# Optimization experiments

Hardware: AMD Instinct MI355X
Metric: run time of the kernel (lower is better)

The kernel has to match this reference:

```python
import jax, jax.numpy as jnp
import numpy as np

H, N, M = 1024, 128, 512
EPS_COS = 1e-8


def setup_inputs() -> dict:
    key = jax.random.key(0)
    ks = iter(jax.random.split(key, 64))
    def rn(shape, s=0.02):
        return jax.random.normal(next(ks), shape, jnp.float32) * s
    x = jax.random.normal(next(ks), (1, H), jnp.float32)
    prw = jax.random.uniform(next(ks), (1, N), jnp.float32)
    prev_read_w = prw / jnp.sum(prw, axis=1, keepdims=True)
    pww = jax.random.uniform(next(ks), (1, N), jnp.float32)
    prev_write_w = pww / jnp.sum(pww, axis=1, keepdims=True)
    inp = {
        "x": x,
        "prev_read_w": prev_read_w,
        "prev_write_w": prev_write_w,
        "h0": rn((1, H), 0.1),
        "c0": rn((1, H), 0.1),
        "memory": jnp.ones((N, M), jnp.float32),
        "W_ih": rn((4 * H, H)), "W_hh": rn((4 * H, H)),
        "b_ih": rn((4 * H,)), "b_hh": rn((4 * H,)),
        "rk_w": rn((M, H)), "rk_b": rn((M,)),
        "rbeta_w": rn((1, H)), "rbeta_b": rn((1,)),
        "rg_w": rn((1, H)), "rg_b": rn((1,)),
        "rs_w": rn((N, H)), "rs_b": rn((N,)),
        "rgamma_w": rn((1, H)), "rgamma_b": rn((1,)),
        "wk_w": rn((M, H)), "wk_b": rn((M,)),
        "wbeta_w": rn((1, H)), "wbeta_b": rn((1,)),
        "wg_w": rn((1, H)), "wg_b": rn((1,)),
        "ws_w": rn((N, H)), "ws_b": rn((N,)),
        "wgamma_w": rn((1, H)), "wgamma_b": rn((1,)),
        "we_w": rn((N * M, H)), "we_b": rn((N * M,)),
        "wa_w": rn((M, H)), "wa_b": rn((M,)),
        "fc_w": rn((H, H + M)), "fc_b": rn((H,)),
    }
    return inp


def _lstm_cell(x, h, c, W_ih, W_hh, b_ih, b_hh):
    # torch gate order: i, f, g, o
    gates = x @ W_ih.T + b_ih + h @ W_hh.T + b_hh  # (1, 4H)
    i, f, g, o = jnp.split(gates, 4, axis=1)
    c_new = jax.nn.sigmoid(f) * c + jax.nn.sigmoid(i) * jnp.tanh(g)
    h_new = jax.nn.sigmoid(o) * jnp.tanh(c_new)
    return h_new, c_new


def _address(x, prev_w, mem, k_w, k_b, beta_w, beta_b, g_w, g_b, s_w, s_b, gamma_w, gamma_b):
    k = x @ k_w.T + k_b                                  # (1, M)
    beta = jax.nn.softplus(x @ beta_w.T + beta_b)        # (1, 1)
    g = jax.nn.sigmoid(x @ g_w.T + g_b)                  # (1, 1)
    s = jax.nn.softmax(x @ s_w.T + s_b, axis=-1)         # (1, N)
    gamma = 1.0 + jax.nn.softplus(x @ gamma_w.T + gamma_b)  # (1, 1)
    # cosine similarity of each memory row with k
    mem_n = jnp.maximum(jnp.linalg.norm(mem, axis=1), EPS_COS)     # (N,)
    k_n = jnp.maximum(jnp.linalg.norm(k[0]), EPS_COS)
    cos = (mem @ k[0]) / (mem_n * k_n)                   # (N,)
    w_c = jax.nn.softmax(beta * cos[None, :], axis=1)    # (1, N)
    w_g = g * w_c + (1.0 - g) * prev_w                   # (1, N)
    # circular convolution: w_t[i] = sum_j w_g[j] * s[(i - j) mod N]
    idx = (jnp.arange(N)[:, None] - jnp.arange(N)[None, :]) % N    # (N, N)
    w_t = (s[0][idx] @ w_g[0])[None, :]                  # (1, N)
    w = w_t ** gamma
    w = w / (jnp.sum(w, axis=1, keepdims=True) + 1e-16)
    return w


def reference(x, prev_read_w, prev_write_w, h0, c0, memory,
              W_ih, W_hh, b_ih, b_hh,
              rk_w, rk_b, rbeta_w, rbeta_b, rg_w, rg_b, rs_w, rs_b, rgamma_w, rgamma_b,
              wk_w, wk_b, wbeta_w, wbeta_b, wg_w, wg_b, ws_w, ws_b, wgamma_w, wgamma_b,
              we_w, we_b, wa_w, wa_b, fc_w, fc_b):
    sg = jax.lax.stop_gradient
    # controller (single LSTM step, batch 1)
    h, c = _lstm_cell(x, h0, c0, W_ih, W_hh, b_ih, b_hh)
    co = h  # controller output (1, H)
    mem = sg(memory)  # memory is detached in the original
    # read head
    rw = _address(co, prev_read_w, mem, rk_w, rk_b, rbeta_w, rbeta_b,
                  rg_w, rg_b, rs_w, rs_b, rgamma_w, rgamma_b)
    read = rw @ mem                                      # (1, M)
    # write head (note: receives prev_read_w, faithful to source)
    ww = _address(co, prev_read_w, mem, wk_w, wk_b, wbeta_w, wbeta_b,
                  wg_w, wg_b, ws_w, ws_b, wgamma_w, wgamma_b)
    e = jax.nn.sigmoid(co @ we_w.T + we_b)               # (1, N*M)
    a = co @ wa_w.T + wa_b                               # (1, M)
    # memory write with detached w, e, a (as in original)
    ww_d, e_d, a_d = sg(ww), sg(e), sg(a)
    new_mem = memory * (1.0 - ww_d @ e_d.reshape(N, M))  # (1,M) broadcast over (N,M)
    new_mem = new_mem + ww_d.T * a_d                     # (N,1)*(1,M)
    # output projection
    fc_in = jnp.concatenate([co, read], axis=1)          # (1, H+M)
    out = fc_in @ fc_w.T + fc_b                          # (1, H)
    return (out, sg(rw), sg(ww), h, c, new_mem)
```

## Files before the change

kernel.cpp:

```cpp
#include <hip/hip_runtime.h>
#include <math.h>

#define HH 1024
#define NN 128
#define MM 512

typedef float vf4 __attribute__((ext_vector_type(4)));

#define OFF_RW 1024
#define OFF_WW 1152
#define OFF_H  1280
#define OFF_C  2304
#define OFF_NM 3328

#define WS_GATES   0
#define WS_MNORM   5120
#define WS_A       5248
#define WS_KR      5760
#define WS_KW      6272
#define WS_RSLOG   6784
#define WS_WSLOG   6912
#define WS_FCPART  7040
#define WS_SCAL    8064
#define WS_WWV     8072
#define WS_RWV     8200
#define WS_ERASE   8328
#define WS_READ    8840

__device__ __forceinline__ float sigmoidf_(float z) { return 1.f / (1.f + expf(-z)); }
__device__ __forceinline__ float softplusf_(float z) {
    return fmaxf(z, 0.f) + log1pf(expf(-fabsf(z)));
}
__device__ __forceinline__ float wave_reduce(float v) {
    #pragma unroll
    for (int off = 32; off > 0; off >>= 1) v += __shfl_down(v, off, 64);
    return v;
}
__device__ __forceinline__ float wave_reduce_max(float v) {
    #pragma unroll
    for (int off = 32; off > 0; off >>= 1) v = fmaxf(v, __shfl_down(v, off, 64));
    return v;
}
__device__ __forceinline__ float block_sum(float v, float* wred, int t) {
    __syncthreads();
    float r = wave_reduce(v);
    if ((t & 63) == 0) wred[t >> 6] = r;
    __syncthreads();
    float s = 0.f;
    #pragma unroll
    for (int i = 0; i < 16; ++i) s += wred[i];
    return s;
}
__device__ __forceinline__ float block_max(float v, float* wred, int t) {
    __syncthreads();
    float r = wave_reduce_max(v);
    if ((t & 63) == 0) wred[t >> 6] = r;
    __syncthreads();
    float s = -1e30f;
    #pragma unroll
    for (int i = 0; i < 16; ++i) s = fmaxf(s, wred[i]);
    return s;
}

__device__ __forceinline__ void recompute_co(
    const float* __restrict__ gates, const float* __restrict__ c0,
    float* s_co, float* __restrict__ out, bool wr, int t)
{
    #pragma unroll
    for (int jj = 0; jj < 4; ++jj) {
        int j = t + jj * 256;
        float gi = gates[j], gf = gates[j + 1024];
        float gg = gates[j + 2048], go = gates[j + 3072];
        float cn = sigmoidf_(gf) * c0[j] + sigmoidf_(gi) * tanhf(gg);
        float hn = sigmoidf_(go) * tanhf(cn);
        s_co[j] = hn;
        if (wr) { out[OFF_H + j] = hn; out[OFF_C + j] = cn; }
    }
    __syncthreads();
}

__global__ __launch_bounds__(256) void k1_gates_norms(
    const float* __restrict__ x, const float* __restrict__ h0,
    const float* __restrict__ W_ih, const float* __restrict__ W_hh,
    const float* __restrict__ b_ih, const float* __restrict__ b_hh,
    const float* __restrict__ memory, float* __restrict__ gates,
    float* __restrict__ mem_norm)
{
    int t = threadIdx.x, lane = t & 63, wv = t >> 6;
    if (blockIdx.x < 1024) {
        int r = blockIdx.x * 4 + wv;
        const vf4* wi = (const vf4*)(W_ih + (long long)r * HH);
        const vf4* wh = (const vf4*)(W_hh + (long long)r * HH);
        const vf4* x4 = (const vf4*)x;
        const vf4* h4 = (const vf4*)h0;
        float acc = 0.f;
        #pragma unroll
        for (int q = 0; q < 4; ++q) {
            vf4 aa = __builtin_nontemporal_load(&wi[q * 64 + lane]);
            vf4 bb = x4[q * 64 + lane];
            acc += aa[0] * bb[0] + aa[1] * bb[1] + aa[2] * bb[2] + aa[3] * bb[3];
        }
        #pragma unroll
        for (int q = 0; q < 4; ++q) {
            vf4 aa = __builtin_nontemporal_load(&wh[q * 64 + lane]);
            vf4 bb = h4[q * 64 + lane];
            acc += aa[0] * bb[0] + aa[1] * bb[1] + aa[2] * bb[2] + aa[3] * bb[3];
        }
        acc = wave_reduce(acc);
        if (lane == 0) gates[r] = acc + b_ih[r] + b_hh[r];
    } else {
        int n = (blockIdx.x - 1024) * 4 + wv;
        const vf4* r4 = (const vf4*)(memory + n * MM);
        float acc = 0.f;
        #pragma unroll
        for (int q = 0; q < 2; ++q) {
            vf4 aa = r4[q * 64 + lane];
            acc += aa[0] * aa[0] + aa[1] * aa[1] + aa[2] * aa[2] + aa[3] * aa[3];
        }
        acc = wave_reduce(acc);
        if (lane == 0) mem_norm[n] = sqrtf(acc);
    }
}

#define K3S_ROWS 2822
__global__ __launch_bounds__(256) void k3_small(
    const float* __restrict__ gates, const float* __restrict__ c0,
    const float* __restrict__ wa_w, const float* __restrict__ wa_b,
    const float* __restrict__ rk_w, const float* __restrict__ rk_b,
    const float* __restrict__ wk_w, const float* __restrict__ wk_b,
    const float* __restrict__ rs_w, const float* __restrict__ rs_b,
    const float* __restrict__ sw_w, const float* __restrict__ sw_b,
    const float* __restrict__ fc_w, const float* __restrict__ fc_b,
    const float* __restrict__ rbeta_w, const float* __restrict__ rbeta_b,
    const float* __restrict__ rg_w, const float* __restrict__ rg_b,
    const float* __restrict__ rgamma_w, const float* __restrict__ rgamma_b,
    const float* __restrict__ wbeta_w, const float* __restrict__ wbeta_b,
    const float* __restrict__ wg_w, const float* __restrict__ wg_b,
    const float* __restrict__ wgamma_w, const float* __restrict__ wgamma_b,
    float* __restrict__ a, float* __restrict__ kr, float* __restrict__ kw,
    float* __restrict__ rs_logit, float* __restrict__ ws_logit,
    float* __restrict__ fc_part, float* __restrict__ scal,
    float* __restrict__ out, float* __restrict__ erase)
{
    __shared__ float s_co[1024];
    int t = threadIdx.x, lane = t & 63, wv = t >> 6;
    bool b0 = (blockIdx.x == 0);
    recompute_co(gates, c0, s_co, out, b0, t);
    if (b0) { erase[t] = 0.f; erase[t + 256] = 0.f; }

    int r = blockIdx.x * 4 + wv;
    if (r >= K3S_ROWS) return;
    const float* row;
    float bias = 0.f;
    float* dst;
    if (r < 512) {
        row = wa_w + (long long)r * HH; if (lane == 0) bias = wa_b[r]; dst = a + r;
    } else if (r < 1024) {
        int i = r - 512; row = rk_w + (long long)i * HH; if (lane == 0) bias = rk_b[i]; dst = kr + i;
    } else if (r < 1536) {
        int i = r - 1024; row = wk_w + (long long)i * HH; if (lane == 0) bias = wk_b[i]; dst = kw + i;
    } else if (r < 1664) {
        int i = r - 1536; row = rs_w + (long long)i * HH; if (lane == 0) bias = rs_b[i]; dst = rs_logit + i;
    } else if (r < 1792) {
        int i = r - 1664; row = sw_w + (long long)i * HH; if (lane == 0) bias = sw_b[i]; dst = ws_logit + i;
    } else if (r < 2816) {
        int i = r - 1792; row = fc_w + (long long)i * 1536; if (lane == 0) bias = fc_b[i]; dst = fc_part + i;
    } else {
        int i = r - 2816;
        const float* wsrc; const float* bsrc;
        switch (i) {
            case 0: wsrc = rbeta_w;  bsrc = rbeta_b;  break;
            case 1: wsrc = rg_w;     bsrc = rg_b;     break;
            case 2: wsrc = rgamma_w; bsrc = rgamma_b; break;
            case 3: wsrc = wbeta_w;  bsrc = wbeta_b;  break;
            case 4: wsrc = wg_w;     bsrc = wg_b;     break;
            default: wsrc = wgamma_w; bsrc = wgamma_b; break;
        }
        row = wsrc; if (lane == 0) bias = bsrc[0]; dst = scal + i;
    }
    const vf4* r4 = (const vf4*)row;
    const vf4* c4 = (const vf4*)s_co;
    float acc = 0.f;
    #pragma unroll
    for (int q = 0; q < 4; ++q) {
        vf4 aa = r4[q * 64 + lane], bb = c4[q * 64 + lane];
        acc += aa[0] * bb[0] + aa[1] * bb[1] + aa[2] * bb[2] + aa[3] * bb[3];
    }
    acc = wave_reduce(acc);
    if (lane == 0) *dst = acc + bias;
}

__global__ __launch_bounds__(1024) void k4_address(
    const float* __restrict__ kr, const float* __restrict__ kw,
    const float* __restrict__ scal,
    const float* __restrict__ rs_logit, const float* __restrict__ ws_logit,
    const float* __restrict__ prev_w, const float* __restrict__ mem_norm,
    const float* __restrict__ memory,
    float* __restrict__ out, float* __restrict__ rwv, float* __restrict__ wwv)
{
    int head = blockIdx.x;
    int t = threadIdx.x, lane = t & 63, wv = t >> 6;
    const float* k = head ? kw : kr;
    const float* slog = head ? ws_logit : rs_logit;
    float beta  = softplusf_(scal[head ? 3 : 0]);
    float gg    = sigmoidf_(scal[head ? 4 : 1]);
    float gamma = 1.f + softplusf_(scal[head ? 5 : 2]);

    __shared__ float wred[16];
    __shared__ float s_cos[128];
    __shared__ float s_s[128];
    __shared__ float s_wg[128];

    float kv = (t < 512) ? k[t] : 0.f;
    float k_norm = sqrtf(block_sum(kv * kv, wred, t));

    const vf4* k4p = (const vf4*)k;
    vf4 bb0 = k4p[lane], bb1 = k4p[64 + lane];
    #pragma unroll
    for (int i = 0; i < 8; ++i) {
        int n = wv * 8 + i;
        const vf4* r4 = (const vf4*)(memory + n * MM);
        vf4 a0 = r4[lane], a1 = r4[64 + lane];
        float acc = a0[0] * bb0[0] + a0[1] * bb0[1] + a0[2] * bb0[2] + a0[3] * bb0[3]
                  + a1[0] * bb1[0] + a1[1] * bb1[1] + a1[2] * bb1[2] + a1[3] * bb1[3];
        acc = wave_reduce(acc);
        if (lane == 0)
            s_cos[n] = acc / (fmaxf(mem_norm[n], 1e-8f) * fmaxf(k_norm, 1e-8f));
    }
    __syncthreads();

    float z = (t < 128) ? beta * s_cos[t] : -1e30f;
    float zmax = block_max(z, wred, t);
    float ez = (t < 128) ? expf(z - zmax) : 0.f;
    float zsum = block_sum(ez, wred, t);
    if (t < 128) s_wg[t] = gg * (ez / zsum) + (1.f - gg) * prev_w[t];

    float sl = (t < 128) ? slog[t] : -1e30f;
    float smax = block_max(sl, wred, t);
    float es = (t < 128) ? expf(sl - smax) : 0.f;
    float ssum = block_sum(es, wred, t);
    if (t < 128) s_s[t] = es / ssum;
    __syncthreads();

    float wt = 0.f;
    if (t < 128) {
        #pragma unroll 8
        for (int j = 0; j < 128; ++j) wt += s_wg[j] * s_s[(t - j) & 127];
        wt = powf(wt, gamma);
    }
    float wsum = block_sum((t < 128) ? wt : 0.f, wred, t);
    if (t < 128) {
        float wf = wt / (wsum + 1e-16f);
        out[(head ? OFF_WW : OFF_RW) + t] = wf;
        (head ? wwv : rwv)[t] = wf;
    }
}

__global__ __launch_bounds__(256) void k5_bige(
    const float* __restrict__ gates, const float* __restrict__ c0,
    const float* __restrict__ we_w, const float* __restrict__ we_b,
    const float* __restrict__ wwv, float* __restrict__ erase,
    const float* __restrict__ rwv, const float* __restrict__ memory,
    float* __restrict__ readv)
{
    __shared__ float s_co[1024];
    int t = threadIdx.x, lane = t & 63, wv = t >> 6;
    int b = blockIdx.x;
    if (b < 4096) {
        recompute_co(gates, c0, s_co, (float*)0, false, t);
        int wid = b * 4 + wv;
        long long r0 = (long long)wid * 4;
        const vf4* c4 = (const vf4*)s_co;
        const float* base = we_w + r0 * HH;
        float acc0 = 0.f, acc1 = 0.f, acc2 = 0.f, acc3 = 0.f;
        #pragma unroll
        for (int q = 0; q < 4; ++q) {
            vf4 bb = c4[q * 64 + lane];
            vf4 a0 = __builtin_nontemporal_load((const vf4*)(base) + q * 64 + lane);
            vf4 a1 = __builtin_nontemporal_load((const vf4*)(base + HH) + q * 64 + lane);
            vf4 a2 = __builtin_nontemporal_load((const vf4*)(base + 2 * HH) + q * 64 + lane);
            vf4 a3 = __builtin_nontemporal_load((const vf4*)(base + 3 * HH) + q * 64 + lane);
            acc0 += a0[0] * bb[0] + a0[1] * bb[1] + a0[2] * bb[2] + a0[3] * bb[3];
            acc1 += a1[0] * bb[0] + a1[1] * bb[1] + a1[2] * bb[2] + a1[3] * bb[3];
            acc2 += a2[0] * bb[0] + a2[1] * bb[1] + a2[2] * bb[2] + a2[3] * bb[3];
            acc3 += a3[0] * bb[0] + a3[1] * bb[1] + a3[2] * bb[2] + a3[3] * bb[3];
        }
        acc0 = wave_reduce(acc0);
        acc1 = wave_reduce(acc1);
        acc2 = wave_reduce(acc2);
        acc3 = wave_reduce(acc3);
        if (lane == 0) {
            int n = (int)(r0 >> 9), m0 = (int)(r0 & 511);
            float wn = wwv[n];
            float e0 = sigmoidf_(acc0 + we_b[r0]);
            float e1 = sigmoidf_(acc1 + we_b[r0 + 1]);
            float e2 = sigmoidf_(acc2 + we_b[r0 + 2]);
            float e3 = sigmoidf_(acc3 + we_b[r0 + 3]);
            atomicAdd(&erase[m0],     wn * e0);
            atomicAdd(&erase[m0 + 1], wn * e1);
            atomicAdd(&erase[m0 + 2], wn * e2);
            atomicAdd(&erase[m0 + 3], wn * e3);
        }
    } else {
        if (t < 128) s_co[t] = rwv[t];
        __syncthreads();
        int m = (b - 4096) * 256 + t;
        float acc = 0.f;
        #pragma unroll 4
        for (int n = 0; n < NN; ++n) acc += s_co[n] * memory[n * MM + m];
        readv[m] = acc;
    }
}

__global__ __launch_bounds__(256) void k6_final(
    const float* __restrict__ memory, const float* __restrict__ erase,
    const float* __restrict__ wwv, const float* __restrict__ a,
    const float* __restrict__ fc_w, const float* __restrict__ fc_part,
    const float* __restrict__ readv, float* __restrict__ out)
{
    int b = blockIdx.x, t = threadIdx.x;
    if (b < 256) {
        int idx = b * 256 + t;
        int n = idx >> 9, m = idx & 511;
        out[OFF_NM + idx] = memory[idx] * (1.f - erase[m]) + wwv[n] * a[m];
    } else {
        int w = (b - 256) * 4 + (t >> 6);
        int lane = t & 63;
        const vf4* r4 = (const vf4*)(fc_w + (long long)w * 1536 + 1024);
        const vf4* v4 = (const vf4*)readv;
        float acc = 0.f;
        #pragma unroll
        for (int q = 0; q < 2; ++q) {
            vf4 aa = r4[q * 64 + lane], bb = v4[q * 64 + lane];
            acc += aa[0] * bb[0] + aa[1] * bb[1] + aa[2] * bb[2] + aa[3] * bb[3];
        }
        acc = wave_reduce(acc);
        if (lane == 0) out[w] = fc_part[w] + acc;
    }
}

extern "C" void kernel_launch(void* const* d_in, const int* in_sizes, int n_in,
                              void* d_out, int out_size, void* d_ws, size_t ws_size,
                              hipStream_t stream)
{
    const float* x           = (const float*)d_in[0];
    const float* prev_read_w = (const float*)d_in[1];
    const float* h0      = (const float*)d_in[3];
    const float* c0      = (const float*)d_in[4];
    const float* memory  = (const float*)d_in[5];
    const float* W_ih    = (const float*)d_in[6];
    const float* W_hh    = (const float*)d_in[7];
    const float* b_ih    = (const float*)d_in[8];
    const float* b_hh    = (const float*)d_in[9];
    const float* rk_w    = (const float*)d_in[10];
    const float* rk_b    = (const float*)d_in[11];
    const float* rbeta_w = (const float*)d_in[12];
    const float* rbeta_b = (const float*)d_in[13];
    const float* rg_w    = (const float*)d_in[14];
    const float* rg_b    = (const float*)d_in[15];
    const float* rs_w    = (const float*)d_in[16];
    const float* rs_b    = (const float*)d_in[17];
    const float* rgamma_w = (const float*)d_in[18];
    const float* rgamma_b = (const float*)d_in[19];
    const float* wk_w    = (const float*)d_in[20];
    const float* wk_b    = (const float*)d_in[21];
    const float* wbeta_w = (const float*)d_in[22];
    const float* wbeta_b = (const float*)d_in[23];
    const float* wg_w    = (const float*)d_in[24];
    const float* wg_b    = (const float*)d_in[25];
    const float* sw_w    = (const float*)d_in[26];
    const float* sw_b    = (const float*)d_in[27];
    const float* wgamma_w = (const float*)d_in[28];
    const float* wgamma_b = (const float*)d_in[29];
    const float* we_w    = (const float*)d_in[30];
    const float* we_b    = (const float*)d_in[31];
    const float* wa_w    = (const float*)d_in[32];
    const float* wa_b    = (const float*)d_in[33];
    const float* fc_w    = (const float*)d_in[34];
    const float* fc_b    = (const float*)d_in[35];

    float* ws  = (float*)d_ws;
    float* out = (float*)d_out;

    float* gates    = ws + WS_GATES;
    float* mem_norm = ws + WS_MNORM;
    float* a        = ws + WS_A;
    float* kr       = ws + WS_KR;
    float* kw       = ws + WS_KW;
    float* rs_logit = ws + WS_RSLOG;
    float* ws_logit = ws + WS_WSLOG;
    float* fc_part  = ws + WS_FCPART;
    float* scal     = ws + WS_SCAL;
    float* wwv      = ws + WS_WWV;
    float* rwv      = ws + WS_RWV;
    float* erase    = ws + WS_ERASE;
    float* readv    = ws + WS_READ;

    k1_gates_norms<<<1056, 256, 0, stream>>>(x, h0, W_ih, W_hh, b_ih, b_hh,
                                             memory, gates, mem_norm);
    k3_small<<<(K3S_ROWS + 3) / 4, 256, 0, stream>>>(
        gates, c0, wa_w, wa_b, rk_w, rk_b, wk_w, wk_b, rs_w, rs_b, sw_w, sw_b,
        fc_w, fc_b,
        rbeta_w, rbeta_b, rg_w, rg_b, rgamma_w, rgamma_b,
        wbeta_w, wbeta_b, wg_w, wg_b, wgamma_w, wgamma_b,
        a, kr, kw, rs_logit, ws_logit, fc_part, scal, out, erase);
    k4_address<<<2, 1024, 0, stream>>>(kr, kw, scal, rs_logit, ws_logit,
                                       prev_read_w, mem_norm, memory,
                                       out, rwv, wwv);
    k5_bige<<<4098, 256, 0, stream>>>(gates, c0, we_w, we_b, wwv, erase,
                                      rwv, memory, readv);
    k6_final<<<512, 256, 0, stream>>>(memory, erase, wwv, a, fc_w, fc_part,
                                      readv, out);
}
```

Measured before the change: 473.1 us.

## Fuse addressing into erase GEMV kernel and store erase vector instead of atomics

The addressing computation now runs as two extra blocks inside the big erase GEMV kernel, which removes the separate k4 launch. The controller output is written once to workspace, so the 4096 erase blocks no longer recompute the LSTM cell. The erase values e are stored in full (N*M) and reduced against ww in the final kernel, which also computes the read vector and the fc read projection, removing the atomics and one launch. In exchange the final kernel reads 256KB of e per block across 128 blocks, and the read/fc blocks each redundantly recompute the read vector.

```diff
diff --git a/kernel.cpp b/kernel.cpp
--- a/kernel.cpp
+++ b/kernel.cpp
@@ -14,6 +14,7 @@
 #define OFF_NM 3328
 
 #define WS_GATES   0
+#define WS_CO      4096
 #define WS_MNORM   5120
 #define WS_A       5248
 #define WS_KR      5760
@@ -24,8 +25,7 @@
 #define WS_SCAL    8064
 #define WS_WWV     8072
 #define WS_RWV     8200
-#define WS_ERASE   8328
-#define WS_READ    8840
+#define WS_E       8320
 
 __device__ __forceinline__ float sigmoidf_(float z) { return 1.f / (1.f + expf(-z)); }
 __device__ __forceinline__ float softplusf_(float z) {
@@ -41,42 +41,19 @@
     for (int off = 32; off > 0; off >>= 1) v = fmaxf(v, __shfl_down(v, off, 64));
     return v;
 }
-__device__ __forceinline__ float block_sum(float v, float* wred, int t) {
+__device__ __forceinline__ float block_sum4(float v, float* wred, int t) {
     __syncthreads();
     float r = wave_reduce(v);
     if ((t & 63) == 0) wred[t >> 6] = r;
     __syncthreads();
-    float s = 0.f;
-    #pragma unroll
-    for (int i = 0; i < 16; ++i) s += wred[i];
-    return s;
-}
-__device__ __forceinline__ float block_max(float v, float* wred, int t) {
+    return wred[0] + wred[1] + wred[2] + wred[3];
+}
+__device__ __forceinline__ float block_max4(float v, float* wred, int t) {
     __syncthreads();
     float r = wave_reduce_max(v);
     if ((t & 63) == 0) wred[t >> 6] = r;
     __syncthreads();
-    float s = -1e30f;
-    #pragma unroll
-    for (int i = 0; i < 16; ++i) s = fmaxf(s, wred[i]);
-    return s;
-}
-
-__device__ __forceinline__ void recompute_co(
-    const float* __restrict__ gates, const float* __restrict__ c0,
-    float* s_co, float* __restrict__ out, bool wr, int t)
-{
-    #pragma unroll
-    for (int jj = 0; jj < 4; ++jj) {
-        int j = t + jj * 256;
-        float gi = gates[j], gf = gates[j + 1024];
-        float gg = gates[j + 2048], go = gates[j + 3072];
-        float cn = sigmoidf_(gf) * c0[j] + sigmoidf_(gi) * tanhf(gg);
-        float hn = sigmoidf_(go) * tanhf(cn);
-        s_co[j] = hn;
-        if (wr) { out[OFF_H + j] = hn; out[OFF_C + j] = cn; }
-    }
-    __syncthreads();
+    return fmaxf(fmaxf(wred[0], wred[1]), fmaxf(wred[2], wred[3]));
 }
 
 __global__ __launch_bounds__(256) void k1_gates_norms(
@@ -140,13 +117,22 @@
     float* __restrict__ a, float* __restrict__ kr, float* __restrict__ kw,
     float* __restrict__ rs_logit, float* __restrict__ ws_logit,
     float* __restrict__ fc_part, float* __restrict__ scal,
-    float* __restrict__ out, float* __restrict__ erase)
+    float* __restrict__ out, float* __restrict__ co_ws)
 {
     __shared__ float s_co[1024];
     int t = threadIdx.x, lane = t & 63, wv = t >> 6;
     bool b0 = (blockIdx.x == 0);
-    recompute_co(gates, c0, s_co, out, b0, t);
-    if (b0) { erase[t] = 0.f; erase[t + 256] = 0.f; }
+    #pragma unroll
+    for (int jj = 0; jj < 4; ++jj) {
+        int j = t + jj * 256;
+        float gi = gates[j], gf = gates[j + 1024];
+        float gg = gates[j + 2048], go = gates[j + 3072];
+        float cn = sigmoidf_(gf) * c0[j] + sigmoidf_(gi) * tanhf(gg);
+        float hn = sigmoidf_(go) * tanhf(cn);
+        s_co[j] = hn;
+        if (b0) { out[OFF_H + j] = hn; out[OFF_C + j] = cn; co_ws[j] = hn; }
+    }
+    __syncthreads();
 
     int r = blockIdx.x * 4 + wv;
     if (r >= K3S_ROWS) return;
@@ -190,7 +176,10 @@
     if (lane == 0) *dst = acc + bias;
 }
 
-__global__ __launch_bounds__(1024) void k4_address(
+__global__ __launch_bounds__(256) void k5_bige(
+    const float* __restrict__ co,
+    const float* __restrict__ we_w, const float* __restrict__ we_b,
+    float* __restrict__ e,
     const float* __restrict__ kr, const float* __restrict__ kw,
     const float* __restrict__ scal,
     const float* __restrict__ rs_logit, const float* __restrict__ ws_logit,
@@ -198,79 +187,12 @@
     const float* __restrict__ memory,
     float* __restrict__ out, float* __restrict__ rwv, float* __restrict__ wwv)
 {
-    int head = blockIdx.x;
-    int t = threadIdx.x, lane = t & 63, wv = t >> 6;
-    const float* k = head ? kw : kr;
-    const float* slog = head ? ws_logit : rs_logit;
-    float beta  = softplusf_(scal[head ? 3 : 0]);
-    float gg    = sigmoidf_(scal[head ? 4 : 1]);
-    float gamma = 1.f + softplusf_(scal[head ? 5 : 2]);
-
-    __shared__ float wred[16];
-    __shared__ float s_cos[128];
-    __shared__ float s_s[128];
-    __shared__ float s_wg[128];
-
-    float kv = (t < 512) ? k[t] : 0.f;
-    float k_norm = sqrtf(block_sum(kv * kv, wred, t));
-
-    const vf4* k4p = (const vf4*)k;
-    vf4 bb0 = k4p[lane], bb1 = k4p[64 + lane];
-    #pragma unroll
-    for (int i = 0; i < 8; ++i) {
-        int n = wv * 8 + i;
-        const vf4* r4 = (const vf4*)(memory + n * MM);
-        vf4 a0 = r4[lane], a1 = r4[64 + lane];
-        float acc = a0[0] * bb0[0] + a0[1] * bb0[1] + a0[2] * bb0[2] + a0[3] * bb0[3]
-                  + a1[0] * bb1[0] + a1[1] * bb1[1] + a1[2] * bb1[2] + a1[3] * bb1[3];
-        acc = wave_reduce(acc);
-        if (lane == 0)
-            s_cos[n] = acc / (fmaxf(mem_norm[n], 1e-8f) * fmaxf(k_norm, 1e-8f));
-    }
-    __syncthreads();
-
-    float z = (t < 128) ? beta * s_cos[t] : -1e30f;
-    float zmax = block_max(z, wred, t);
-    float ez = (t < 128) ? expf(z - zmax) : 0.f;
-    float zsum = block_sum(ez, wred, t);
-    if (t < 128) s_wg[t] = gg * (ez / zsum) + (1.f - gg) * prev_w[t];
-
-    float sl = (t < 128) ? slog[t] : -1e30f;
-    float smax = block_max(sl, wred, t);
-    float es = (t < 128) ? expf(sl - smax) : 0.f;
-    float ssum = block_sum(es, wred, t);
-    if (t < 128) s_s[t] = es / ssum;
-    __syncthreads();
-
-    float wt = 0.f;
-    if (t < 128) {
-        #pragma unroll 8
-        for (int j = 0; j < 128; ++j) wt += s_wg[j] * s_s[(t - j) & 127];
-        wt = powf(wt, gamma);
-    }
-    float wsum = block_sum((t < 128) ? wt : 0.f, wred, t);
-    if (t < 128) {
-        float wf = wt / (wsum + 1e-16f);
-        out[(head ? OFF_WW : OFF_RW) + t] = wf;
-        (head ? wwv : rwv)[t] = wf;
-    }
-}
-
-__global__ __launch_bounds__(256) void k5_bige(
-    const float* __restrict__ gates, const float* __restrict__ c0,
-    const float* __restrict__ we_w, const float* __restrict__ we_b,
-    const float* __restrict__ wwv, float* __restrict__ erase,
-    const float* __restrict__ rwv, const float* __restrict__ memory,
-    float* __restrict__ readv)
-{
-    __shared__ float s_co[1024];
     int t = threadIdx.x, lane = t & 63, wv = t >> 6;
     int b = blockIdx.x;
-    if (b < 4096) {
-        recompute_co(gates, c0, s_co, (float*)0, false, t);
-        int wid = b * 4 + wv;
+    if (b >= 2) {
+        int wid = (b - 2) * 4 + wv;
         long long r0 = (long long)wid * 4;
-        const vf4* c4 = (const vf4*)s_co;
+        const vf4* c4 = (const vf4*)co;
         const float* base = we_w + r0 * HH;
         float acc0 = 0.f, acc1 = 0.f, acc2 = 0.f, acc3 = 0.f;
         #pragma unroll
@@ -290,52 +212,123 @@
         acc2 = wave_reduce(acc2);
         acc3 = wave_reduce(acc3);
         if (lane == 0) {
-            int n = (int)(r0 >> 9), m0 = (int)(r0 & 511);
-            float wn = wwv[n];
-            float e0 = sigmoidf_(acc0 + we_b[r0]);
-            float e1 = sigmoidf_(acc1 + we_b[r0 + 1]);
-            float e2 = sigmoidf_(acc2 + we_b[r0 + 2]);
-            float e3 = sigmoidf_(acc3 + we_b[r0 + 3]);
-            atomicAdd(&erase[m0],     wn * e0);
-            atomicAdd(&erase[m0 + 1], wn * e1);
-            atomicAdd(&erase[m0 + 2], wn * e2);
-            atomicAdd(&erase[m0 + 3], wn * e3);
+            vf4 ev;
+            ev[0] = sigmoidf_(acc0 + we_b[r0]);
+            ev[1] = sigmoidf_(acc1 + we_b[r0 + 1]);
+            ev[2] = sigmoidf_(acc2 + we_b[r0 + 2]);
+            ev[3] = sigmoidf_(acc3 + we_b[r0 + 3]);
+            *(vf4*)(e + r0) = ev;
+        }
+        return;
+    }
+
+    int head = b;
+    const float* k = head ? kw : kr;
+    const float* slog = head ? ws_logit : rs_logit;
+    float beta  = softplusf_(scal[head ? 3 : 0]);
+    float gg    = sigmoidf_(scal[head ? 4 : 1]);
+    float gamma = 1.f + softplusf_(scal[head ? 5 : 2]);
+
+    __shared__ float wred[4];
+    __shared__ float s_cos[128];
+    __shared__ float s_s[128];
+    __shared__ float s_wg[128];
+
+    float a0 = k[t], a1 = k[t + 256];
+    float k_norm = sqrtf(block_sum4(a0 * a0 + a1 * a1, wred, t));
+
+    const vf4* k4p = (const vf4*)k;
+    vf4 bb0 = k4p[lane], bb1 = k4p[64 + lane];
+    for (int i = 0; i < 32; ++i) {
+        int n = wv * 32 + i;
+        const vf4* r4 = (const vf4*)(memory + n * MM);
+        vf4 m0 = r4[lane], m1 = r4[64 + lane];
+        float acc = m0[0] * bb0[0] + m0[1] * bb0[1] + m0[2] * bb0[2] + m0[3] * bb0[3]
+                  + m1[0] * bb1[0] + m1[1] * bb1[1] + m1[2] * bb1[2] + m1[3] * bb1[3];
+        acc = wave_reduce(acc);
+        if (lane == 0)
+            s_cos[n] = acc / (fmaxf(mem_norm[n], 1e-8f) * fmaxf(k_norm, 1e-8f));
+    }
+    __syncthreads();
+
+    float z = (t < 128) ? beta * s_cos[t] : -1e30f;
+    float zmax = block_max4(z, wred, t);
+    float ez = (t < 128) ? expf(z - zmax) : 0.f;
+    float zsum = block_sum4(ez, wred, t);
+    if (t < 128) s_wg[t] = gg * (ez / zsum) + (1.f - gg) * prev_w[t];
+
+    float sl = (t < 128) ? slog[t] : -1e30f;
+    float smax = block_max4(sl, wred, t);
+    float es = (t < 128) ? expf(sl - smax) : 0.f;
+    float ssum = block_sum4(es, wred, t);
+    if (t < 128) s_s[t] = es / ssum;
+    __syncthreads();
+
+    float wt = 0.f;
+    if (t < 128) {
+        #pragma unroll 8
+        for (int j = 0; j < 128; ++j) wt += s_wg[j] * s_s[(t - j) & 127];
+        wt = powf(wt, gamma);
+    }
+    float wsum = block_sum4((t < 128) ? wt : 0.f, wred, t);
+    if (t < 128) {
+        float wf = wt / (wsum + 1e-16f);
+        out[(head ? OFF_WW : OFF_RW) + t] = wf;
+        (head ? wwv : rwv)[t] = wf;
+    }
+}
+
+__global__ __launch_bounds__(256) void k6_final(
+    const float* __restrict__ memory, const float* __restrict__ e,
+    const float* __restrict__ wwv, const float* __restrict__ rwv,
+    const float* __restrict__ a,
+    const float* __restrict__ fc_w, const float* __restrict__ fc_part,
+    float* __restrict__ out)
+{
+    int b = blockIdx.x, t = threadIdx.x, lane = t & 63, wv = t >> 6;
+    if (b < 128) {
+        int n = b;
+        __shared__ float s_ww[128];
+        if (t < 128) s_ww[t] = wwv[t];
+        __syncthreads();
+        float wn = s_ww[n];
+        #pragma unroll
+        for (int half = 0; half < 2; ++half) {
+            int m = t + half * 256;
+            float er = 0.f;
+            #pragma unroll 4
+            for (int j = 0; j < NN; ++j) er += s_ww[j] * e[j * MM + m];
+            int idx = n * MM + m;
+            out[OFF_NM + idx] = memory[idx] * (1.f - er) + wn * a[m];
         }
     } else {
-        if (t < 128) s_co[t] = rwv[t];
+        __shared__ float s_rw[128];
+        __shared__ float s_rv[512];
+        if (t < 128) s_rw[t] = rwv[t];
         __syncthreads();
-        int m = (b - 4096) * 256 + t;
-        float acc = 0.f;
-        #pragma unroll 4
-        for (int n = 0; n < NN; ++n) acc += s_co[n] * memory[n * MM + m];
-        readv[m] = acc;
-    }
-}
-
-__global__ __launch_bounds__(256) void k6_final(
-    const float* __restrict__ memory, const float* __restrict__ erase,
-    const float* __restrict__ wwv, const float* __restrict__ a,
-    const float* __restrict__ fc_w, const float* __restrict__ fc_part,
-    const float* __restrict__ readv, float* __restrict__ out)
-{
-    int b = blockIdx.x, t = threadIdx.x;
-    if (b < 256) {
-        int idx = b * 256 + t;
-        int n = idx >> 9, m = idx & 511;
-        out[OFF_NM + idx] = memory[idx] * (1.f - erase[m]) + wwv[n] * a[m];
-    } else {
-        int w = (b - 256) * 4 + (t >> 6);
-        int lane = t & 63;
-        const vf4* r4 = (const vf4*)(fc_w + (long long)w * 1536 + 1024);
-        const vf4* v4 = (const vf4*)readv;
-        float acc = 0.f;
-        #pragma unroll
-        for (int q = 0; q < 2; ++q) {
-            vf4 aa = r4[q * 64 + lane], bb = v4[q * 64 + lane];
-            acc += aa[0] * bb[0] + aa[1] * bb[1] + aa[2] * bb[2] + aa[3] * bb[3];
-        }
-        acc = wave_reduce(acc);
-        if (lane == 0) out[w] = fc_part[w] + acc;
+        #pragma unroll
+        for (int half = 0; half < 2; ++half) {
+            int m = t + half * 256;
+            float acc = 0.f;
+            #pragma unroll 4
+            for (int n = 0; n < NN; ++n) acc += s_rw[n] * memory[n * MM + m];
+            s_rv[m] = acc;
+        }
+        __syncthreads();
+        const vf4* v4 = (const vf4*)s_rv;
+        #pragma unroll
+        for (int i = 0; i < 8; ++i) {
+            int w = (b - 128) * 32 + wv * 8 + i;
+            const vf4* r4 = (const vf4*)(fc_w + (long long)w * 1536 + 1024);
+            float acc = 0.f;
+            #pragma unroll
+            for (int q = 0; q < 2; ++q) {
+                vf4 aa = r4[q * 64 + lane], bb = v4[q * 64 + lane];
+                acc += aa[0] * bb[0] + aa[1] * bb[1] + aa[2] * bb[2] + aa[3] * bb[3];
+            }
+            acc = wave_reduce(acc);
+            if (lane == 0) out[w] = fc_part[w] + acc;
+        }
     }
 }
 
@@ -383,6 +376,7 @@
     float* out = (float*)d_out;
 
     float* gates    = ws + WS_GATES;
+    float* co       = ws + WS_CO;
     float* mem_norm = ws + WS_MNORM;
     float* a        = ws + WS_A;
     float* kr       = ws + WS_KR;
@@ -393,8 +387,7 @@
     float* scal     = ws + WS_SCAL;
     float* wwv      = ws + WS_WWV;
     float* rwv      = ws + WS_RWV;
-    float* erase    = ws + WS_ERASE;
-    float* readv    = ws + WS_READ;
+    float* e        = ws + WS_E;
 
     k1_gates_norms<<<1056, 256, 0, stream>>>(x, h0, W_ih, W_hh, b_ih, b_hh,
                                              memory, gates, mem_norm);
@@ -403,12 +396,11 @@
         fc_w, fc_b,
         rbeta_w, rbeta_b, rg_w, rg_b, rgamma_w, rgamma_b,
         wbeta_w, wbeta_b, wg_w, wg_b, wgamma_w, wgamma_b,
-        a, kr, kw, rs_logit, ws_logit, fc_part, scal, out, erase);
-    k4_address<<<2, 1024, 0, stream>>>(kr, kw, scal, rs_logit, ws_logit,
-                                       prev_read_w, mem_norm, memory,
-                                       out, rwv, wwv);
-    k5_bige<<<4098, 256, 0, stream>>>(gates, c0, we_w, we_b, wwv, erase,
-                                      rwv, memory, readv);
-    k6_final<<<512, 256, 0, stream>>>(memory, erase, wwv, a, fc_w, fc_part,
-                                      readv, out);
-}
+        a, kr, kw, rs_logit, ws_logit, fc_part, scal, out, co);
+    k5_bige<<<4098, 256, 0, stream>>>(co, we_w, we_b, e,
+                                      kr, kw, scal, rs_logit, ws_logit,
+                                      prev_read_w, mem_norm, memory,
+                                      out, rwv, wwv);
+    k6_final<<<160, 256, 0, stream>>>(memory, e, wwv, rwv, a,
+                                      fc_w, fc_part, out);
+}
```

Result: no change. 474.2 us (+0.2%).
